# Kernel optimization log

Hardware: AMD Instinct MI355X
Metric: run time of the kernel (lower is better)

Reference implementation:

```python
import jax, jax.numpy as jnp
import numpy as np

B, L, D, H = 2, 2048, 2048, 16
HD = D // H           # head_dim = 128
HD2 = HD // 2         # rotary pair count = 64


def setup_inputs() -> dict:
    key = jax.random.key(0)
    ks = jax.random.split(key, 6)
    x = jax.random.normal(ks[0], (B, L, D), dtype=jnp.float32)
    # RoPE angles: theta_i = 10000^(-2i/HD), angles[l, i] = l * theta_i
    inv_freq = 1.0 / (10000.0 ** (np.arange(0, HD, 2, dtype=np.float32) / HD))
    angles = np.arange(L, dtype=np.float32)[:, None] * inv_freq[None, :]  # [L, HD2]
    freqs_cos = jnp.asarray(np.cos(angles))[None]  # [1, L, HD2]
    freqs_sin = jnp.asarray(np.sin(angles))[None]  # [1, L, HD2]
    s = 1.0 / np.sqrt(D)
    Wq = jax.random.normal(ks[1], (D, D), dtype=jnp.float32) * s
    Wk = jax.random.normal(ks[2], (D, D), dtype=jnp.float32) * s
    Wv = jax.random.normal(ks[3], (D, D), dtype=jnp.float32) * s
    Wo = jax.random.normal(ks[4], (D, D), dtype=jnp.float32) * s
    return {"x": x, "freqs_cos": freqs_cos, "freqs_sin": freqs_sin,
            "Wq": Wq, "Wk": Wk, "Wv": Wv, "Wo": Wo}


def _apply_rope(t, cos, sin):
    # t: [B, H, L, HD]; cos/sin: [1, L, HD2] -> broadcast as [1, 1, L, HD2]
    t2 = t.reshape(*t.shape[:-1], HD2, 2)
    t0, t1 = t2[..., 0], t2[..., 1]
    c = cos[:, None]
    s = sin[:, None]
    r0 = t0 * c - t1 * s
    r1 = t0 * s + t1 * c
    return jnp.stack([r0, r1], axis=-1).reshape(t.shape)


def reference(x, freqs_cos, freqs_sin, Wq, Wk, Wv, Wo):
    b, l, d = x.shape
    # projections (torch Linear: x @ W.T)
    Q = (x @ Wq.T).reshape(b, l, H, HD).transpose(0, 2, 1, 3)  # [b,h,l,hd]
    K = (x @ Wk.T).reshape(b, l, H, HD).transpose(0, 2, 1, 3)
    V = (x @ Wv.T).reshape(b, l, H, HD).transpose(0, 2, 1, 3)
    Q = _apply_rope(Q, freqs_cos[:, :l], freqs_sin[:, :l])
    K = _apply_rope(K, freqs_cos[:, :l], freqs_sin[:, :l])
    scale = 1.0 / jnp.sqrt(jnp.asarray(HD, dtype=x.dtype))
    scores = jnp.einsum('bhqd,bhkd->bhqk', Q, K) * scale  # [b,h,l,l]
    causal = jnp.tril(jnp.ones((l, l), dtype=bool))
    scores = jnp.where(causal, scores, jnp.finfo(scores.dtype).min)
    probs = jax.nn.softmax(scores, axis=-1)
    out = jnp.einsum('bhqk,bhkd->bhqd', probs, V)  # [b,h,l,hd]
    out = out.transpose(0, 2, 1, 3).reshape(b, l, d)
    return out @ Wo.T
```

## Files before the change

kernel.cpp:

```cpp
#include <hip/hip_runtime.h>
#include <cstdint>
#include <cstddef>

typedef float f32x4 __attribute__((ext_vector_type(4)));
typedef short bf16x8 __attribute__((ext_vector_type(8)));
typedef short bf16x4 __attribute__((ext_vector_type(4)));
typedef unsigned int u32x4 __attribute__((ext_vector_type(4)));

#define LOG2E 1.4426950408889634f
#define K2E 0.12750102296293331f
#define MFMA_BF16 __builtin_amdgcn_mfma_f32_16x16x32_bf16

__device__ inline float bf2f(short s) {
  return (float)__builtin_bit_cast(__bf16, s);
}
__device__ inline short f2bf(float f) {
  return __builtin_bit_cast(short, (__bf16)f);
}
__device__ inline unsigned f2bfu(float f) {
  return (unsigned)__builtin_bit_cast(unsigned short, (__bf16)f);
}

__device__ inline void gload_lds16(const void* g, void* l) {
  __builtin_amdgcn_global_load_lds(
      (const __attribute__((address_space(1))) void*)g,
      (__attribute__((address_space(3))) void*)l, 16, 0, 0);
}

__global__ __launch_bounds__(256) void cvt_all(const float* __restrict__ x,
                                               const float* __restrict__ w0,
                                               const float* __restrict__ w1,
                                               const float* __restrict__ w2,
                                               const float* __restrict__ w3,
                                               __bf16* __restrict__ out) {
  int i = (blockIdx.x * 256 + threadIdx.x) * 8;
  const float* s;
  int off;
  if (i < 8388608) {
    s = x; off = i;
  } else {
    int j = i - 8388608;
    int sel = j >> 22;
    s = (sel == 0) ? w0 : (sel == 1) ? w1 : (sel == 2) ? w2 : w3;
    off = j & 4194303;
  }
  f32x4 a = *(const f32x4*)(s + off);
  f32x4 b = *(const f32x4*)(s + off + 4);
  bf16x8 r;
#pragma unroll
  for (int j = 0; j < 4; ++j) {
    r[j]     = f2bf(a[j]);
    r[j + 4] = f2bf(b[j]);
  }
  *(bf16x8*)(out + i) = r;
}

__device__ inline void stage_half(const __bf16* __restrict__ gbase, int K,
                                  int k0, char* ldsHalf, int wid, int lane) {
#pragma unroll
  for (int j = 0; j < 2; ++j) {
    int idx = (wid * 2 + j) * 64 + lane;
    int row = idx >> 3;
    int c16 = (idx & 7) ^ (row & 7);
    gload_lds16(gbase + (size_t)row * K + k0 + c16 * 8,
                ldsHalf + (wid * 2 + j) * 1024);
  }
}

__device__ inline bf16x8 lds_frag(const char* halfbase, int row, int ks, int g) {
  return *(const bf16x8*)(halfbase + row * 128 + ((((ks << 2) | g) ^ (row & 7)) << 4));
}

#define WAITV(n) asm volatile("s_waitcnt vmcnt(" #n ")" ::: "memory")

template <bool OUT_F32, bool ROPE>
__global__ __launch_bounds__(512, 1) void gemm128(const __bf16* __restrict__ A,
                                                  const __bf16* __restrict__ B,
                                                  void* __restrict__ Cv,
                                                  const float* __restrict__ fc,
                                                  const float* __restrict__ fs,
                                                  int M, int N, int K) {
  __shared__ __attribute__((aligned(128))) char lds[147456];
  const int tid = threadIdx.x, wid = tid >> 6, lane = tid & 63;
  const int g = lane >> 4, lc = lane & 15;
  const int wm = wid >> 2, wn = wid & 3;

  const int gx = gridDim.x;
  int nwg = gx * gridDim.y;
  int bid = blockIdx.y * gx + blockIdx.x;
  int cpx = nwg >> 3;
  int swz = (bid & 7) * cpx + (bid >> 3);
  const int bx = swz % gx, by = swz / gx;

  const __bf16* Ag = A + (size_t)(by * 128) * K;
  const __bf16* Bg = B + (size_t)(bx * 256) * K;
  const __bf16* Bg1 = Bg + 128 * (size_t)K;
  const int NT = K >> 6;

  f32x4 acc[2][4][2];
#pragma unroll
  for (int hb = 0; hb < 2; ++hb)
#pragma unroll
    for (int m = 0; m < 4; ++m)
#pragma unroll
      for (int n = 0; n < 2; ++n) acc[hb][m][n] = f32x4{0.f, 0.f, 0.f, 0.f};

  stage_half(Ag,  K, 0,  lds + 0,             wid, lane);
  stage_half(Bg,  K, 0,  lds + 49152,         wid, lane);
  stage_half(Bg1, K, 0,  lds + 98304,         wid, lane);
  stage_half(Ag,  K, 64, lds + 16384,         wid, lane);
  stage_half(Bg,  K, 64, lds + 49152 + 16384, wid, lane);
  stage_half(Bg1, K, 64, lds + 98304 + 16384, wid, lane);
  WAITV(8);
  __builtin_amdgcn_s_barrier();

  bf16x8 a[4][2], b0[2][2], b1[2][2];
  int sc = 0;

  for (int T = 0; T < NT; ++T) {
    char* As  = lds + sc * 16384;
    char* B0s = lds + 49152 + sc * 16384;
    char* B1s = lds + 98304 + sc * 16384;
    int s2 = sc + 2; if (s2 >= 3) s2 -= 3;
    char* As2  = lds + s2 * 16384;
    char* B0s2 = lds + 49152 + s2 * 16384;
    char* B1s2 = lds + 98304 + s2 * 16384;
    const int k2 = (T + 2) << 6;

#pragma unroll
    for (int m = 0; m < 4; ++m)
#pragma unroll
      for (int ks = 0; ks < 2; ++ks)
        a[m][ks] = lds_frag(As, wm * 64 + m * 16 + lc, ks, g);
#pragma unroll
    for (int n = 0; n < 2; ++n)
#pragma unroll
      for (int ks = 0; ks < 2; ++ks)
        b0[n][ks] = lds_frag(B0s, wn * 32 + n * 16 + lc, ks, g);
    if (T + 2 < NT) {
      stage_half(Ag, K, k2, As2, wid, lane);
      stage_half(Bg, K, k2, B0s2, wid, lane);
      WAITV(10);
    } else if (T + 1 < NT) {
      WAITV(6);
    } else {
      WAITV(0);
    }
    __builtin_amdgcn_s_barrier();
    __builtin_amdgcn_s_setprio(1);
#pragma unroll
    for (int m = 0; m < 4; ++m)
#pragma unroll
      for (int n = 0; n < 2; ++n) {
        acc[0][m][n] = MFMA_BF16(a[m][0], b0[n][0], acc[0][m][n], 0, 0, 0);
        acc[0][m][n] = MFMA_BF16(a[m][1], b0[n][1], acc[0][m][n], 0, 0, 0);
      }
    __builtin_amdgcn_s_setprio(0);

#pragma unroll
    for (int n = 0; n < 2; ++n)
#pragma unroll
      for (int ks = 0; ks < 2; ++ks)
        b1[n][ks] = lds_frag(B1s, wn * 32 + n * 16 + lc, ks, g);
    if (T + 2 < NT) {
      stage_half(Bg1, K, k2, B1s2, wid, lane);
      WAITV(8);
    } else if (T + 1 < NT) {
      WAITV(2);
    }
    __builtin_amdgcn_s_barrier();
    __builtin_amdgcn_s_setprio(1);
#pragma unroll
    for (int m = 0; m < 4; ++m)
#pragma unroll
      for (int n = 0; n < 2; ++n) {
        acc[1][m][n] = MFMA_BF16(a[m][0], b1[n][0], acc[1][m][n], 0, 0, 0);
        acc[1][m][n] = MFMA_BF16(a[m][1], b1[n][1], acc[1][m][n], 0, 0, 0);
      }
    __builtin_amdgcn_s_setprio(0);

    sc = (sc + 1 == 3) ? 0 : sc + 1;
  }

  if (ROPE && bx < 16) {
#pragma unroll
    for (int m = 0; m < 4; ++m)
#pragma unroll
      for (int r = 0; r < 4; ++r) {
        int l = (by * 128 + wm * 64 + m * 16 + g * 4 + r) & 2047;
#pragma unroll
        for (int n = 0; n < 2; ++n) {
          int i0 = (wn * 32 + n * 16 + lc) >> 1;
          float c = fc[l * 64 + i0];
          float s = fs[l * 64 + i0];
#pragma unroll
          for (int hb = 0; hb < 2; ++hb) {
            float v = acc[hb][m][n][r];
            float pv = __shfl_xor(v, 1);
            acc[hb][m][n][r] = (lc & 1) ? (pv * s + v * c) : (v * c - pv * s);
          }
        }
      }
  }

#pragma unroll
  for (int hb = 0; hb < 2; ++hb)
#pragma unroll
    for (int m = 0; m < 4; ++m)
#pragma unroll
      for (int n = 0; n < 2; ++n)
#pragma unroll
        for (int r = 0; r < 4; ++r) {
          int rr = by * 128 + wm * 64 + m * 16 + g * 4 + r;
          int cc = bx * 256 + hb * 128 + wn * 32 + n * 16 + lc;
          if (OUT_F32)
            ((float*)Cv)[(size_t)rr * N + cc] = acc[hb][m][n][r];
          else
            ((__bf16*)Cv)[(size_t)rr * N + cc] = (__bf16)acc[hb][m][n][r];
        }
}

__global__ void transpose_v(const __bf16* __restrict__ qkv, __bf16* __restrict__ vt) {
  __shared__ __bf16 tile[32][33];
  const int b = blockIdx.z;
  const int l0 = blockIdx.x * 32, c0 = blockIdx.y * 32;
  for (int i = threadIdx.y; i < 32; i += 8)
    tile[i][threadIdx.x] = qkv[(size_t)(b * 2048 + l0 + i) * 6144 + 4096 + c0 + threadIdx.x];
  __syncthreads();
  for (int i = threadIdx.y; i < 32; i += 8)
    vt[(size_t)b * 4194304 + (size_t)(c0 + i) * 2048 + l0 + threadIdx.x] = tile[threadIdx.x][i];
}

__device__ __forceinline__ void attn_segment(const __bf16* __restrict__ qkv,
                                             const __bf16* __restrict__ vt,
                                             __bf16* __restrict__ aout,
                                             int b, int h, int bh,
                                             int qseg0, int nt,
                                             char* smem, int tid) {
  const int wid = tid >> 6, lane = tid & 63;
  const int g = lane >> 4, lc = lane & 15;
  const int q0w = qseg0 + wid * 16;
  const float k2e = K2E;

  bf16x8 qreg[4];
  {
    const __bf16* qp = qkv + (size_t)(b * 2048 + q0w + lc) * 6144 + h * 128 + g * 8;
#pragma unroll
    for (int c = 0; c < 4; ++c) qreg[c] = *(const bf16x8*)(qp + c * 32);
  }

  f32x4 oaccT[8];
#pragma unroll
  for (int dc = 0; dc < 8; ++dc) oaccT[dc] = f32x4{0.f, 0.f, 0.f, 0.f};
  float m_run = -1e30f, l_run = 0.f;

  const int rK = tid >> 2, sK = tid & 3;
  const int dbase = tid >> 3, sg = tid & 7;
  const __bf16* kb = qkv + (size_t)(b * 2048) * 6144 + 2048 + h * 128;
  const __bf16* vb = vt + (size_t)bh * 262144;

  bf16x8 kreg[4], vreg[4];
  {
    const __bf16* kg = kb + (size_t)rK * 6144 + sK * 8;
#pragma unroll
    for (int kk = 0; kk < 4; ++kk) kreg[kk] = *(const bf16x8*)(kg + kk * 32);
    const __bf16* vg = vb + sg * 8;
#pragma unroll
    for (int kk = 0; kk < 4; ++kk)
      vreg[kk] = *(const bf16x8*)(vg + (size_t)(dbase + kk * 32) * 2048);
  }

  __syncthreads();

  for (int t = 0; t < nt; ++t) {
    const int kv0 = t * 64;
    char* Ks = smem + (t & 1) * 16384;
    char* Vs = smem + 32768 + (t & 1) * 16384;

#pragma unroll
    for (int kk = 0; kk < 4; ++kk)
      *(bf16x8*)(Ks + rK * 256 + ((sK * 16 + kk * 64) ^ ((rK & 7) << 4))) = kreg[kk];
#pragma unroll
    for (int kk = 0; kk < 4; ++kk) {
      int d = dbase + kk * 32;
      *(bf16x8*)(Vs + d * 128 + ((sg * 16) ^ ((d & 7) << 4))) = vreg[kk];
    }
    __syncthreads();

    if (t + 1 < nt) {
      const __bf16* kg = kb + (size_t)(kv0 + 64 + rK) * 6144 + sK * 8;
#pragma unroll
      for (int kk = 0; kk < 4; ++kk) kreg[kk] = *(const bf16x8*)(kg + kk * 32);
      const __bf16* vg = vb + kv0 + 64 + sg * 8;
#pragma unroll
      for (int kk = 0; kk < 4; ++kk)
        vreg[kk] = *(const bf16x8*)(vg + (size_t)(dbase + kk * 32) * 2048);
    }

    f32x4 sacc[4];
#pragma unroll
    for (int kc = 0; kc < 4; ++kc) sacc[kc] = f32x4{0.f, 0.f, 0.f, 0.f};
#pragma unroll
    for (int kc = 0; kc < 4; ++kc) {
      const int kr = kc * 16 + lc;
#pragma unroll
      for (int c = 0; c < 4; ++c) {
        bf16x8 kf = *(const bf16x8*)(Ks + kr * 256 + ((c * 64 + g * 16) ^ ((kr & 7) << 4)));
        sacc[kc] = MFMA_BF16(kf, qreg[c], sacc[kc], 0, 0, 0);
      }
    }

    if (kv0 + 63 > q0w) {
#pragma unroll
      for (int kc = 0; kc < 4; ++kc)
#pragma unroll
        for (int r = 0; r < 4; ++r)
          if (kv0 + kc * 16 + g * 4 + r > q0w + lc) sacc[kc][r] = -1e30f;
    }

    float mx = sacc[0][0];
#pragma unroll
    for (int kc = 0; kc < 4; ++kc)
#pragma unroll
      for (int r = 0; r < 4; ++r) mx = fmaxf(mx, sacc[kc][r]);
    mx = fmaxf(mx, __shfl_xor(mx, 16));
    mx = fmaxf(mx, __shfl_xor(mx, 32));
    float mn = fmaxf(m_run, mx);
    float al = exp2f((m_run - mn) * k2e);
    m_run = mn;
    float p[4][4];
    float ls = 0.f;
#pragma unroll
    for (int kc = 0; kc < 4; ++kc)
#pragma unroll
      for (int r = 0; r < 4; ++r) {
        p[kc][r] = exp2f((sacc[kc][r] - mn) * k2e);
        ls += p[kc][r];
      }
    ls += __shfl_xor(ls, 16);
    ls += __shfl_xor(ls, 32);
    l_run = l_run * al + ls;
#pragma unroll
    for (int dc = 0; dc < 8; ++dc)
#pragma unroll
      for (int r = 0; r < 4; ++r) oaccT[dc][r] *= al;

    unsigned pk[4][2];
#pragma unroll
    for (int kc = 0; kc < 4; ++kc)
#pragma unroll
      for (int hh = 0; hh < 2; ++hh)
        pk[kc][hh] = f2bfu(p[kc][2 * hh]) | (f2bfu(p[kc][2 * hh + 1]) << 16);

    const int sA = (g & 1) * 32 + lc, sB = sA + 16;
    const bool hi = (g >> 1) != 0;
    bf16x8 brg[2];
#pragma unroll
    for (int c = 0; c < 2; ++c) {
      unsigned a0 = (unsigned)__shfl((int)pk[2 * c][0], sA);
      unsigned b0v = (unsigned)__shfl((int)pk[2 * c + 1][0], sA);
      unsigned a1 = (unsigned)__shfl((int)pk[2 * c][1], sA);
      unsigned b1v = (unsigned)__shfl((int)pk[2 * c + 1][1], sA);
      unsigned a2 = (unsigned)__shfl((int)pk[2 * c][0], sB);
      unsigned b2v = (unsigned)__shfl((int)pk[2 * c + 1][0], sB);
      unsigned a3 = (unsigned)__shfl((int)pk[2 * c][1], sB);
      unsigned b3v = (unsigned)__shfl((int)pk[2 * c + 1][1], sB);
      u32x4 wv;
      wv[0] = hi ? b0v : a0;
      wv[1] = hi ? b1v : a1;
      wv[2] = hi ? b2v : a2;
      wv[3] = hi ? b3v : a3;
      brg[c] = __builtin_bit_cast(bf16x8, wv);
    }

#pragma unroll
    for (int dc = 0; dc < 8; ++dc) {
      const int vr = dc * 16 + lc;
      bf16x8 vf0 = *(const bf16x8*)(Vs + vr * 128 + ((g * 16) ^ ((vr & 7) << 4)));
      bf16x8 vf1 = *(const bf16x8*)(Vs + vr * 128 + ((64 + g * 16) ^ ((vr & 7) << 4)));
      oaccT[dc] = MFMA_BF16(vf0, brg[0], oaccT[dc], 0, 0, 0);
      oaccT[dc] = MFMA_BF16(vf1, brg[1], oaccT[dc], 0, 0, 0);
    }
  }

  {
    float inv = 1.f / l_run;
    __bf16* op = aout + (size_t)(b * 2048 + q0w + lc) * 2048 + h * 128 + g * 4;
#pragma unroll
    for (int dc = 0; dc < 8; ++dc) {
      bf16x4 o;
#pragma unroll
      for (int r = 0; r < 4; ++r) o[r] = f2bf(oaccT[dc][r] * inv);
      *(bf16x4*)(op + dc * 16) = o;
    }
  }
}

__global__ __launch_bounds__(256, 2) void flash_attn(const __bf16* __restrict__ qkv,
                                                     const __bf16* __restrict__ vt,
                                                     __bf16* __restrict__ aout) {
  __shared__ __attribute__((aligned(16))) char smem[65536];
  const int tid = threadIdx.x;
  const int j = blockIdx.x;
  const int bh = blockIdx.y, b = bh >> 4, h = bh & 15;

  attn_segment(qkv, vt, aout, b, h, bh, j * 64, j + 1, smem, tid);
  attn_segment(qkv, vt, aout, b, h, bh, (31 - j) * 64, 32 - j, smem, tid);
}

extern "C" void kernel_launch(void* const* d_in, const int* in_sizes, int n_in,
                              void* d_out, int out_size, void* d_ws, size_t ws_size,
                              hipStream_t stream) {
  const float* x    = (const float*)d_in[0];
  const float* fcos = (const float*)d_in[1];
  const float* fsin = (const float*)d_in[2];
  const float* Wq   = (const float*)d_in[3];
  const float* Wk   = (const float*)d_in[4];
  const float* Wv   = (const float*)d_in[5];
  const float* Wo   = (const float*)d_in[6];

  char* ws = (char*)d_ws;
  __bf16* xb   = (__bf16*)(ws);
  __bf16* Wqkv = (__bf16*)(ws + 16777216);
  __bf16* Wob  = (__bf16*)(ws + 41943040);
  __bf16* QKV  = (__bf16*)(ws + 50331648);
  __bf16* Vt   = (__bf16*)(ws + 100663296);
  __bf16* aout = (__bf16*)(ws + 117440512);
  float* out = (float*)d_out;

  cvt_all<<<12288, 256, 0, stream>>>(x, Wq, Wk, Wv, Wo, xb);

  gemm128<false, true><<<dim3(24, 32), 512, 0, stream>>>(xb, Wqkv, QKV, fcos, fsin,
                                                         4096, 6144, 2048);
  transpose_v<<<dim3(64, 64, 2), dim3(32, 8), 0, stream>>>(QKV, Vt);
  flash_attn<<<dim3(16, 32), 256, 0, stream>>>(QKV, Vt, aout);
  gemm128<true, false><<<dim3(8, 32), 512, 0, stream>>>(aout, Wob, out, nullptr, nullptr,
                                                        4096, 2048, 2048);
}
```

Baseline: 268.1 us.

## Deepen K/V register prefetch to two tiles and raise wave priority around MFMAs

```diff
diff --git a/kernel.cpp b/kernel.cpp
--- a/kernel.cpp
+++ b/kernel.cpp
@@ -231,6 +231,31 @@
     vt[(size_t)b * 4194304 + (size_t)(c0 + i) * 2048 + l0 + threadIdx.x] = tile[threadIdx.x][i];
 }
 
+__device__ __forceinline__ void load_kv(const __bf16* kb, const __bf16* vb,
+                                        int tile, int rK, int sK, int dbase,
+                                        int sg, bf16x8* kreg, bf16x8* vreg) {
+  const __bf16* kg = kb + (size_t)(tile * 64 + rK) * 6144 + sK * 8;
+#pragma unroll
+  for (int kk = 0; kk < 4; ++kk) kreg[kk] = *(const bf16x8*)(kg + kk * 32);
+  const __bf16* vg = vb + tile * 64 + sg * 8;
+#pragma unroll
+  for (int kk = 0; kk < 4; ++kk)
+    vreg[kk] = *(const bf16x8*)(vg + (size_t)(dbase + kk * 32) * 2048);
+}
+
+__device__ __forceinline__ void store_kv(char* Ks, char* Vs, int rK, int sK,
+                                         int dbase, int sg,
+                                         const bf16x8* kreg, const bf16x8* vreg) {
+#pragma unroll
+  for (int kk = 0; kk < 4; ++kk)
+    *(bf16x8*)(Ks + rK * 256 + ((sK * 16 + kk * 64) ^ ((rK & 7) << 4))) = kreg[kk];
+#pragma unroll
+  for (int kk = 0; kk < 4; ++kk) {
+    int d = dbase + kk * 32;
+    *(bf16x8*)(Vs + d * 128 + ((sg * 16) ^ ((d & 7) << 4))) = vreg[kk];
+  }
+}
+
 __device__ __forceinline__ void attn_segment(const __bf16* __restrict__ qkv,
                                              const __bf16* __restrict__ vt,
                                              __bf16* __restrict__ aout,
@@ -259,16 +284,9 @@
   const __bf16* kb = qkv + (size_t)(b * 2048) * 6144 + 2048 + h * 128;
   const __bf16* vb = vt + (size_t)bh * 262144;
 
-  bf16x8 kreg[4], vreg[4];
-  {
-    const __bf16* kg = kb + (size_t)rK * 6144 + sK * 8;
-#pragma unroll
-    for (int kk = 0; kk < 4; ++kk) kreg[kk] = *(const bf16x8*)(kg + kk * 32);
-    const __bf16* vg = vb + sg * 8;
-#pragma unroll
-    for (int kk = 0; kk < 4; ++kk)
-      vreg[kk] = *(const bf16x8*)(vg + (size_t)(dbase + kk * 32) * 2048);
-  }
+  bf16x8 kregA[4], vregA[4], kregB[4], vregB[4];
+  load_kv(kb, vb, 0, rK, sK, dbase, sg, kregA, vregA);
+  load_kv(kb, vb, (nt > 1) ? 1 : 0, rK, sK, dbase, sg, kregB, vregB);
 
   __syncthreads();
 
@@ -277,29 +295,20 @@
     char* Ks = smem + (t & 1) * 16384;
     char* Vs = smem + 32768 + (t & 1) * 16384;
 
-#pragma unroll
-    for (int kk = 0; kk < 4; ++kk)
-      *(bf16x8*)(Ks + rK * 256 + ((sK * 16 + kk * 64) ^ ((rK & 7) << 4))) = kreg[kk];
-#pragma unroll
-    for (int kk = 0; kk < 4; ++kk) {
-      int d = dbase + kk * 32;
-      *(bf16x8*)(Vs + d * 128 + ((sg * 16) ^ ((d & 7) << 4))) = vreg[kk];
-    }
-    __syncthreads();
-
-    if (t + 1 < nt) {
-      const __bf16* kg = kb + (size_t)(kv0 + 64 + rK) * 6144 + sK * 8;
-#pragma unroll
-      for (int kk = 0; kk < 4; ++kk) kreg[kk] = *(const bf16x8*)(kg + kk * 32);
-      const __bf16* vg = vb + kv0 + 64 + sg * 8;
-#pragma unroll
-      for (int kk = 0; kk < 4; ++kk)
-        vreg[kk] = *(const bf16x8*)(vg + (size_t)(dbase + kk * 32) * 2048);
+    if ((t & 1) == 0) {
+      store_kv(Ks, Vs, rK, sK, dbase, sg, kregA, vregA);
+      asm volatile("s_waitcnt lgkmcnt(0)\n\ts_barrier" ::: "memory");
+      if (t + 2 < nt) load_kv(kb, vb, t + 2, rK, sK, dbase, sg, kregA, vregA);
+    } else {
+      store_kv(Ks, Vs, rK, sK, dbase, sg, kregB, vregB);
+      asm volatile("s_waitcnt lgkmcnt(0)\n\ts_barrier" ::: "memory");
+      if (t + 2 < nt) load_kv(kb, vb, t + 2, rK, sK, dbase, sg, kregB, vregB);
     }
 
     f32x4 sacc[4];
 #pragma unroll
     for (int kc = 0; kc < 4; ++kc) sacc[kc] = f32x4{0.f, 0.f, 0.f, 0.f};
+    __builtin_amdgcn_s_setprio(1);
 #pragma unroll
     for (int kc = 0; kc < 4; ++kc) {
       const int kr = kc * 16 + lc;
@@ -309,6 +318,7 @@
         sacc[kc] = MFMA_BF16(kf, qreg[c], sacc[kc], 0, 0, 0);
       }
     }
+    __builtin_amdgcn_s_setprio(0);
 
     if (kv0 + 63 > q0w) {
 #pragma unroll
@@ -373,6 +383,7 @@
       brg[c] = __builtin_bit_cast(bf16x8, wv);
     }
 
+    __builtin_amdgcn_s_setprio(1);
 #pragma unroll
     for (int dc = 0; dc < 8; ++dc) {
       const int vr = dc * 16 + lc;
@@ -381,6 +392,7 @@
       oaccT[dc] = MFMA_BF16(vf0, brg[0], oaccT[dc], 0, 0, 0);
       oaccT[dc] = MFMA_BF16(vf1, brg[1], oaccT[dc], 0, 0, 0);
     }
+    __builtin_amdgcn_s_setprio(0);
   }
 
   {
```

Result: slower. 278.4 us (+3.8%).
